# Performance work log

Hardware: AMD Instinct MI355X
Metric: run time of the kernel (lower is better)

Reference implementation:

```python
import jax, jax.numpy as jnp
import numpy as np

DIM = 96
K = 3
STRIDE = 1
PAD = 1
RED = 4
BN_EPS = 1e-5


def setup_inputs() -> dict:
    key = jax.random.key(0)
    ks = jax.random.split(key, 8)
    b, c, h, w = 32, DIM, 128, 128
    cr = DIM // RED
    return {
        "x": jax.random.normal(ks[0], (b, c, h, w), jnp.float32),
        "w1": jax.random.normal(ks[1], (cr, c), jnp.float32) * 0.1,          # conv1 1x1, no bias
        "gamma": jnp.ones((cr,), jnp.float32),
        "beta": jnp.zeros((cr,), jnp.float32),
        "running_mean": jax.random.normal(ks[2], (cr,), jnp.float32) * 0.1,
        "running_var": jax.random.uniform(ks[3], (cr,), jnp.float32, 0.5, 1.5),
        "w2": jax.random.normal(ks[4], (DIM * K * K, cr), jnp.float32) * 0.1,  # conv2 1x1
        "b2": jax.random.normal(ks[5], (DIM * K * K,), jnp.float32) * 0.1,
        "bias": jnp.zeros((DIM,), jnp.float32),
    }


def _dynamic_weight(x, w1, gamma, beta, running_mean, running_var, w2, b2):
    # AdaptiveAvgPool2d((1,1)) -> [b, c]
    pooled = jnp.mean(x, axis=(2, 3))
    # conv1 (1x1, no bias) on 1x1 spatial == matmul
    h1 = pooled @ w1.T  # [b, c//r]
    # BatchNorm2d in inference mode (running stats)
    h1 = (h1 - running_mean) * jax.lax.rsqrt(running_var + BN_EPS) * gamma + beta
    h1 = jax.nn.sigmoid(h1)
    # conv2 (1x1) == matmul + bias -> [b, dim*k*k]
    wdyn = h1 @ w2.T + b2
    return wdyn.reshape(x.shape[0], DIM, K, K)


def _per_sample_depthwise(x, weight, bias):
    # x: [b, c, h, w], weight: [b, c, k, k] -> per-sample depthwise conv
    def one(xi, wi):
        # xi: [c,h,w], wi: [c,k,k]
        out = jax.lax.conv_general_dilated(
            xi[None], wi[:, None],
            window_strides=(STRIDE, STRIDE),
            padding=[(PAD, PAD), (PAD, PAD)],
            dimension_numbers=("NCHW", "OIHW", "NCHW"),
            feature_group_count=DIM,
        )
        return out[0]

    y = jax.vmap(one)(x, weight)  # [b, c, h', w']
    return y + bias[None, :, None, None]


def reference(x, w1, gamma, beta, running_mean, running_var, w2, b2, bias):
    weight = _dynamic_weight(x, w1, gamma, beta, running_mean, running_var, w2, b2)
    return _per_sample_depthwise(x, weight, bias)
```

## Files before the change

kernel.cpp:

```cpp
#include <hip/hip_runtime.h>
#include <math.h>

#define C_DIM 96
#define CR 24
#define H_DIM 128
#define W_DIM 128
#define B_DIM 32
#define CHUNKS 4
#define ROWS_PER_CHUNK (H_DIM / CHUNKS)

__global__ void pool_kernel(const float* __restrict__ x, float* __restrict__ pooled) {
    int plane = blockIdx.x;
    const float4* xp = (const float4*)(x + (size_t)plane * (H_DIM * W_DIM));
    float s = 0.f;
    for (int i = threadIdx.x; i < 4096; i += 256) {
        float4 v = xp[i];
        s += v.x + v.y + v.z + v.w;
    }
    for (int off = 32; off; off >>= 1) s += __shfl_down(s, off, 64);
    __shared__ float ls[4];
    int lane = threadIdx.x & 63, wv = threadIdx.x >> 6;
    if (lane == 0) ls[wv] = s;
    __syncthreads();
    if (threadIdx.x == 0) {
        float t = ls[0] + ls[1] + ls[2] + ls[3];
        pooled[plane] = t * (1.f / (H_DIM * W_DIM));
    }
}

__global__ void wdyn_kernel(const float* __restrict__ pooled,
                            const float* __restrict__ w1,
                            const float* __restrict__ gamma,
                            const float* __restrict__ beta,
                            const float* __restrict__ rmean,
                            const float* __restrict__ rvar,
                            const float* __restrict__ w2,
                            const float* __restrict__ b2,
                            float* __restrict__ wdyn) {
    int b = blockIdx.x;
    int tid = threadIdx.x;
    __shared__ float pl[C_DIM];
    __shared__ float h1[CR];
    if (tid < C_DIM) pl[tid] = pooled[b * C_DIM + tid];
    __syncthreads();
    if (tid < CR) {
        float s = 0.f;
        const float* wr = w1 + tid * C_DIM;
        for (int c = 0; c < C_DIM; c++) s += pl[c] * wr[c];
        s = (s - rmean[tid]) * rsqrtf(rvar[tid] + 1e-5f) * gamma[tid] + beta[tid];
        h1[tid] = 1.f / (1.f + expf(-s));
    }
    __syncthreads();
    for (int o = tid; o < C_DIM * 9; o += 256) {
        float s = b2[o];
        const float* wr = w2 + o * CR;
        #pragma unroll
        for (int j = 0; j < CR; j++) s += h1[j] * wr[j];
        wdyn[b * (C_DIM * 9) + o] = s;
    }
}

__global__ void __launch_bounds__(256) dwconv_kernel(const float* __restrict__ x,
                                                     const float* __restrict__ wdyn,
                                                     const float* __restrict__ bias,
                                                     float* __restrict__ out) {
    int T = blockIdx.x * 256 + threadIdx.x;
    int g = T & 31;
    int chunk = (T >> 5) & 3;
    int plane = T >> 7;
    int c = plane % C_DIM;
    int col = g << 2;
    int r0 = chunk * ROWS_PER_CHUNK;

    const float* xp = x + (size_t)plane * (H_DIM * W_DIM);
    float* op = out + (size_t)plane * (H_DIM * W_DIM);
    const float* wp = wdyn + (size_t)plane * 9;
    float w00 = wp[0], w01 = wp[1], w02 = wp[2];
    float w10 = wp[3], w11 = wp[4], w12 = wp[5];
    float w20 = wp[6], w21 = wp[7], w22 = wp[8];
    float bb = bias[c];
    const bool leftEdge = (g == 0), rightEdge = (g == 31);

    float4 pv, cv, nv;
    float pl, pr, cl, cr_, nl, nr;

    {
        int r = r0 - 1;
        float4 v;
        if (r >= 0) v = *(const float4*)(xp + r * W_DIM + col);
        else { v.x = v.y = v.z = v.w = 0.f; }
        float l = __shfl_up(v.w, 1, 64);
        float rr = __shfl_down(v.x, 1, 64);
        pv = v; pl = leftEdge ? 0.f : l; pr = rightEdge ? 0.f : rr;
    }
    {
        float4 v = *(const float4*)(xp + r0 * W_DIM + col);
        float l = __shfl_up(v.w, 1, 64);
        float rr = __shfl_down(v.x, 1, 64);
        cv = v; cl = leftEdge ? 0.f : l; cr_ = rightEdge ? 0.f : rr;
    }

    #pragma unroll 4
    for (int i = 0; i < ROWS_PER_CHUNK; i++) {
        int r = r0 + i;
        float4 v;
        if (r + 1 < H_DIM) v = *(const float4*)(xp + (r + 1) * W_DIM + col);
        else { v.x = v.y = v.z = v.w = 0.f; }
        float l = __shfl_up(v.w, 1, 64);
        float rr = __shfl_down(v.x, 1, 64);
        nv = v; nl = leftEdge ? 0.f : l; nr = rightEdge ? 0.f : rr;

        float4 o;
        o.x = w00 * pl   + w01 * pv.x + w02 * pv.y
            + w10 * cl   + w11 * cv.x + w12 * cv.y
            + w20 * nl   + w21 * nv.x + w22 * nv.y + bb;
        o.y = w00 * pv.x + w01 * pv.y + w02 * pv.z
            + w10 * cv.x + w11 * cv.y + w12 * cv.z
            + w20 * nv.x + w21 * nv.y + w22 * nv.z + bb;
        o.z = w00 * pv.y + w01 * pv.z + w02 * pv.w
            + w10 * cv.y + w11 * cv.z + w12 * cv.w
            + w20 * nv.y + w21 * nv.z + w22 * nv.w + bb;
        o.w = w00 * pv.z + w01 * pv.w + w02 * pr
            + w10 * cv.z + w11 * cv.w + w12 * cr_
            + w20 * nv.z + w21 * nv.w + w22 * nr + bb;
        *(float4*)(op + r * W_DIM + col) = o;

        pv = cv; pl = cl; pr = cr_;
        cv = nv; cl = nl; cr_ = nr;
    }
}

extern "C" void kernel_launch(void* const* d_in, const int* in_sizes, int n_in,
                              void* d_out, int out_size, void* d_ws, size_t ws_size,
                              hipStream_t stream) {
    const float* x     = (const float*)d_in[0];
    const float* w1    = (const float*)d_in[1];
    const float* gamma = (const float*)d_in[2];
    const float* beta  = (const float*)d_in[3];
    const float* rmean = (const float*)d_in[4];
    const float* rvar  = (const float*)d_in[5];
    const float* w2    = (const float*)d_in[6];
    const float* b2    = (const float*)d_in[7];
    const float* bias  = (const float*)d_in[8];
    float* out = (float*)d_out;

    float* pooled = (float*)d_ws;
    float* wdyn   = pooled + B_DIM * C_DIM;

    pool_kernel<<<B_DIM * C_DIM, 256, 0, stream>>>(x, pooled);
    wdyn_kernel<<<B_DIM, 256, 0, stream>>>(pooled, w1, gamma, beta, rmean, rvar, w2, b2, wdyn);
    int total_threads = B_DIM * C_DIM * CHUNKS * (W_DIM / 4);
    dwconv_kernel<<<total_threads / 256, 256, 0, stream>>>(x, wdyn, bias, out);
}
```

Before: 396.1 us.

## Fuse dynamic weight MLP into depthwise conv kernel and use nontemporal stores

Removes the separate wdyn kernel launch. Each dwconv block, which covers two planes of one sample, now recomputes the pooled-to-hidden MLP and the 18 dynamic weights plus bias into shared memory before convolving. Output stores become nontemporal so the written planes do not evict x from cache. In exchange, every block redoes the 24x96 hidden-layer matvec (1536 times instead of 32) and adds two barriers before the stencil starts.

```diff
diff --git a/kernel.cpp b/kernel.cpp
--- a/kernel.cpp
+++ b/kernel.cpp
@@ -8,6 +8,8 @@
 #define B_DIM 32
 #define CHUNKS 4
 #define ROWS_PER_CHUNK (H_DIM / CHUNKS)
+
+typedef float nfloat4 __attribute__((ext_vector_type(4)));
 
 __global__ void pool_kernel(const float* __restrict__ x, float* __restrict__ pooled) {
     int plane = blockIdx.x;
@@ -28,61 +30,70 @@
     }
 }
 
-__global__ void wdyn_kernel(const float* __restrict__ pooled,
-                            const float* __restrict__ w1,
-                            const float* __restrict__ gamma,
-                            const float* __restrict__ beta,
-                            const float* __restrict__ rmean,
-                            const float* __restrict__ rvar,
-                            const float* __restrict__ w2,
-                            const float* __restrict__ b2,
-                            float* __restrict__ wdyn) {
-    int b = blockIdx.x;
+__global__ void __launch_bounds__(256) fused_dwconv_kernel(const float* __restrict__ x,
+                                                           const float* __restrict__ pooled,
+                                                           const float* __restrict__ w1,
+                                                           const float* __restrict__ gamma,
+                                                           const float* __restrict__ beta,
+                                                           const float* __restrict__ rmean,
+                                                           const float* __restrict__ rvar,
+                                                           const float* __restrict__ w2,
+                                                           const float* __restrict__ b2,
+                                                           const float* __restrict__ bias,
+                                                           float* __restrict__ out) {
     int tid = threadIdx.x;
+    int plane0 = blockIdx.x * 2;
+    int b = plane0 / C_DIM;
+    int c0 = plane0 % C_DIM;
+
     __shared__ float pl[C_DIM];
     __shared__ float h1[CR];
+    __shared__ float wsm[2][10];
+
     if (tid < C_DIM) pl[tid] = pooled[b * C_DIM + tid];
     __syncthreads();
     if (tid < CR) {
         float s = 0.f;
         const float* wr = w1 + tid * C_DIM;
+        #pragma unroll 8
         for (int c = 0; c < C_DIM; c++) s += pl[c] * wr[c];
         s = (s - rmean[tid]) * rsqrtf(rvar[tid] + 1e-5f) * gamma[tid] + beta[tid];
         h1[tid] = 1.f / (1.f + expf(-s));
     }
     __syncthreads();
-    for (int o = tid; o < C_DIM * 9; o += 256) {
-        float s = b2[o];
-        const float* wr = w2 + o * CR;
-        #pragma unroll
-        for (int j = 0; j < CR; j++) s += h1[j] * wr[j];
-        wdyn[b * (C_DIM * 9) + o] = s;
+    if (tid < 20) {
+        if (tid < 18) {
+            int p = tid / 9, k = tid % 9;
+            int row = (c0 + p) * 9 + k;
+            float s = b2[row];
+            const float* wr = w2 + row * CR;
+            #pragma unroll
+            for (int j = 0; j < CR; j++) s += h1[j] * wr[j];
+            wsm[p][k] = s;
+        } else {
+            wsm[tid - 18][9] = bias[c0 + (tid - 18)];
+        }
     }
-}
+    __syncthreads();
 
-__global__ void __launch_bounds__(256) dwconv_kernel(const float* __restrict__ x,
-                                                     const float* __restrict__ wdyn,
-                                                     const float* __restrict__ bias,
-                                                     float* __restrict__ out) {
-    int T = blockIdx.x * 256 + threadIdx.x;
-    int g = T & 31;
-    int chunk = (T >> 5) & 3;
-    int plane = T >> 7;
-    int c = plane % C_DIM;
+    int g = tid & 31;
+    int chunk = (tid >> 5) & 3;
+    int p = tid >> 7;
+    int plane = plane0 + p;
     int col = g << 2;
     int r0 = chunk * ROWS_PER_CHUNK;
 
     const float* xp = x + (size_t)plane * (H_DIM * W_DIM);
     float* op = out + (size_t)plane * (H_DIM * W_DIM);
-    const float* wp = wdyn + (size_t)plane * 9;
-    float w00 = wp[0], w01 = wp[1], w02 = wp[2];
-    float w10 = wp[3], w11 = wp[4], w12 = wp[5];
-    float w20 = wp[6], w21 = wp[7], w22 = wp[8];
-    float bb = bias[c];
+    const float* wv = wsm[p];
+    float w00 = wv[0], w01 = wv[1], w02 = wv[2];
+    float w10 = wv[3], w11 = wv[4], w12 = wv[5];
+    float w20 = wv[6], w21 = wv[7], w22 = wv[8];
+    float bb = wv[9];
     const bool leftEdge = (g == 0), rightEdge = (g == 31);
 
     float4 pv, cv, nv;
-    float pl, pr, cl, cr_, nl, nr;
+    float plh, prh, clh, crh, nlh, nrh;
 
     {
         int r = r0 - 1;
@@ -91,13 +102,13 @@
         else { v.x = v.y = v.z = v.w = 0.f; }
         float l = __shfl_up(v.w, 1, 64);
         float rr = __shfl_down(v.x, 1, 64);
-        pv = v; pl = leftEdge ? 0.f : l; pr = rightEdge ? 0.f : rr;
+        pv = v; plh = leftEdge ? 0.f : l; prh = rightEdge ? 0.f : rr;
     }
     {
         float4 v = *(const float4*)(xp + r0 * W_DIM + col);
         float l = __shfl_up(v.w, 1, 64);
         float rr = __shfl_down(v.x, 1, 64);
-        cv = v; cl = leftEdge ? 0.f : l; cr_ = rightEdge ? 0.f : rr;
+        cv = v; clh = leftEdge ? 0.f : l; crh = rightEdge ? 0.f : rr;
     }
 
     #pragma unroll 4
@@ -108,25 +119,25 @@
         else { v.x = v.y = v.z = v.w = 0.f; }
         float l = __shfl_up(v.w, 1, 64);
         float rr = __shfl_down(v.x, 1, 64);
-        nv = v; nl = leftEdge ? 0.f : l; nr = rightEdge ? 0.f : rr;
+        nv = v; nlh = leftEdge ? 0.f : l; nrh = rightEdge ? 0.f : rr;
 
-        float4 o;
-        o.x = w00 * pl   + w01 * pv.x + w02 * pv.y
-            + w10 * cl   + w11 * cv.x + w12 * cv.y
-            + w20 * nl   + w21 * nv.x + w22 * nv.y + bb;
+        nfloat4 o;
+        o.x = w00 * plh  + w01 * pv.x + w02 * pv.y
+            + w10 * clh  + w11 * cv.x + w12 * cv.y
+            + w20 * nlh  + w21 * nv.x + w22 * nv.y + bb;
         o.y = w00 * pv.x + w01 * pv.y + w02 * pv.z
             + w10 * cv.x + w11 * cv.y + w12 * cv.z
             + w20 * nv.x + w21 * nv.y + w22 * nv.z + bb;
         o.z = w00 * pv.y + w01 * pv.z + w02 * pv.w
             + w10 * cv.y + w11 * cv.z + w12 * cv.w
             + w20 * nv.y + w21 * nv.z + w22 * nv.w + bb;
-        o.w = w00 * pv.z + w01 * pv.w + w02 * pr
-            + w10 * cv.z + w11 * cv.w + w12 * cr_
-            + w20 * nv.z + w21 * nv.w + w22 * nr + bb;
-        *(float4*)(op + r * W_DIM + col) = o;
+        o.w = w00 * pv.z + w01 * pv.w + w02 * prh
+            + w10 * cv.z + w11 * cv.w + w12 * crh
+            + w20 * nv.z + w21 * nv.w + w22 * nrh + bb;
+        __builtin_nontemporal_store(o, (nfloat4*)(op + r * W_DIM + col));
 
-        pv = cv; pl = cl; pr = cr_;
-        cv = nv; cl = nl; cr_ = nr;
+        pv = cv; plh = clh; prh = crh;
+        cv = nv; clh = nlh; crh = nrh;
     }
 }
 
@@ -145,10 +156,8 @@
     float* out = (float*)d_out;
 
     float* pooled = (float*)d_ws;
-    float* wdyn   = pooled + B_DIM * C_DIM;
 
     pool_kernel<<<B_DIM * C_DIM, 256, 0, stream>>>(x, pooled);
-    wdyn_kernel<<<B_DIM, 256, 0, stream>>>(pooled, w1, gamma, beta, rmean, rvar, w2, b2, wdyn);
-    int total_threads = B_DIM * C_DIM * CHUNKS * (W_DIM / 4);
-    dwconv_kernel<<<total_threads / 256, 256, 0, stream>>>(x, wdyn, bias, out);
+    fused_dwconv_kernel<<<B_DIM * C_DIM / 2, 256, 0, stream>>>(
+        x, pooled, w1, gamma, beta, rmean, rvar, w2, b2, bias, out);
 }
```

Measured after the change: 387.6 us. -2.1%, faster.
